# Kernel optimization log

Hardware: AMD Instinct MI355X
Metric: run time of the kernel (lower is better)

Reference implementation:

```python
import jax, jax.numpy as jnp
import numpy as np

# Module hyperparameters (from init_kwargs)
P = 96                 # num_of_patches
W = 1536.0             # input width
H = 1536.0             # input height
XPS = W / P            # x patch size = 16
YPS = H / P            # y patch size = 16
PROB_THR = 0.9
IOU_THR = 0.5
N = P * P              # total candidate boxes


def setup_inputs() -> dict:
    key = jax.random.key(0)
    # x: [5, P, P] -> channel 0 = probability, 1..4 = (x, y, w, h) in [0,1)
    x = jax.random.uniform(key, (5, P, P), dtype=jnp.float32)
    return {"x": x}


def _pairwise_iou(b):
    # b: [N, 4] xyxy
    x1, y1, x2, y2 = b[:, 0], b[:, 1], b[:, 2], b[:, 3]
    area = (x2 - x1) * (y2 - y1)                       # [N]
    ix1 = jnp.maximum(x1[:, None], x1[None, :])
    iy1 = jnp.maximum(y1[:, None], y1[None, :])
    ix2 = jnp.minimum(x2[:, None], x2[None, :])
    iy2 = jnp.minimum(y2[:, None], y2[None, :])
    inter = jnp.clip(ix2 - ix1, 0.0) * jnp.clip(iy2 - iy1, 0.0)
    union = area[:, None] + area[None, :] - inter
    return jnp.where(union > 0, inter / union, 0.0)    # [N, N]


def _forward(x):
    # --- scale_batch_bbx_xywh, applied densely (invalid entries are masked later) ---
    p = x[0]
    ii = jnp.arange(P, dtype=x.dtype)[:, None]   # row index i
    jj = jnp.arange(P, dtype=x.dtype)[None, :]   # col index j
    bx = x[1] * XPS + ii * XPS
    by = x[2] * YPS + jj * YPS
    bw = x[3] * W
    bh = x[4] * H
    bbx = jnp.stack([p, bx, by, bw, bh], axis=0).reshape(5, N).T   # [N, 5] (p, x, y, w, h)

    # --- remove_low_probability_bbx: fixed-shape validity mask instead of filtering ---
    scores = bbx[:, 0]
    valid = scores > PROB_THR

    # --- convert_batch_to_xyxy + round ---
    x1 = jnp.round(bbx[:, 1])
    y1 = jnp.round(bbx[:, 2])
    x2 = jnp.round(bbx[:, 3] + bbx[:, 1])
    y2 = jnp.round(bbx[:, 4] + bbx[:, 2])

    # --- greedy NMS (torchvision semantics): sort by score desc, suppress by IoU ---
    sort_key = jnp.where(valid, scores, -jnp.inf)
    order = jnp.argsort(-sort_key)
    boxes = jnp.stack([x1, y1, x2, y2], axis=1)[order]   # [N, 4] sorted
    sc = scores[order]
    v = valid[order]
    iou = _pairwise_iou(boxes)                           # [N, N]

    def body(kept, i):
        suppressed = jnp.any(kept & (iou[i] > IOU_THR))
        ki = v[i] & ~suppressed
        return kept.at[i].set(ki), ki

    _, keeps = jax.lax.scan(body, jnp.zeros((N,), bool), jnp.arange(N))

    # --- cat([scores, bbx]) then convert_batch_to_xywh on kept rows ---
    out = jnp.stack(
        [sc, boxes[:, 0], boxes[:, 1], boxes[:, 2] - boxes[:, 0], boxes[:, 3] - boxes[:, 1]],
        axis=1,
    )  # [N, 5] = (score, x, y, w, h), score-descending order like nms output
    out = jnp.where(keeps[:, None], out, 0.0)
    return out, keeps


def reference(x):
    # Returns (out [N,5], keep_mask [N]); rows with keep_mask=False are zeroed.
    # This is the fixed-shape equivalent of the variable-length torch output.
    return _forward(x)
```

## Files before the change

kernel.cpp:

```cpp
#include <hip/hip_runtime.h>

#define PP 96
#define NB (PP*PP)
#define NCH (NB/64)
#define PROB_THR 0.9f
#define FAST_CAP 1024
#define LSTRIDE 1034

typedef unsigned long long u64;
typedef unsigned int u32;

__device__ __forceinline__ void decode_core(int n, float xv, float yv, float wv, float hv,
                                            float& X1, float& Y1, float& X2, float& Y2)
{
    int i = n / PP;
    int j = n - i * PP;
    float bx = __fadd_rn(__fmul_rn(xv, 16.0f), (float)i * 16.0f);
    float by = __fadd_rn(__fmul_rn(yv, 16.0f), (float)j * 16.0f);
    float bw = __fmul_rn(wv, 1536.0f);
    float bh = __fmul_rn(hv, 1536.0f);
    X1 = rintf(bx);
    Y1 = rintf(by);
    X2 = rintf(__fadd_rn(bw, bx));
    Y2 = rintf(__fadd_rn(bh, by));
}

__device__ __forceinline__ void decode_box(const float* __restrict__ x, int n,
                                           float& X1, float& Y1, float& X2, float& Y2)
{
    decode_core(n, x[NB + n], x[2 * NB + n], x[3 * NB + n], x[4 * NB + n], X1, Y1, X2, Y2);
}

__device__ __forceinline__ int iou_hit_nodiv(float ix1, float iy1, float ix2, float iy2, float iar,
                                             float jx1, float jy1, float jx2, float jy2, float jar)
{
    float xx1 = fmaxf(ix1, jx1), yy1 = fmaxf(iy1, jy1);
    float xx2 = fminf(ix2, jx2), yy2 = fminf(iy2, jy2);
    float iw = fmaxf(__fsub_rn(xx2, xx1), 0.0f);
    float ih = fmaxf(__fsub_rn(yy2, yy1), 0.0f);
    float inter = __fmul_rn(iw, ih);
    float uni = __fsub_rn(__fadd_rn(iar, jar), inter);
    return (uni > 0.0f && __fadd_rn(inter, inter) > uni) ? 1 : 0;
}

__device__ __forceinline__ int iou_hit_div(float ix1, float iy1, float ix2, float iy2, float iar,
                                           float jx1, float jy1, float jx2, float jy2, float jar)
{
    float xx1 = fmaxf(ix1, jx1), yy1 = fmaxf(iy1, jy1);
    float xx2 = fminf(ix2, jx2), yy2 = fminf(iy2, jy2);
    float iw = fmaxf(__fsub_rn(xx2, xx1), 0.0f);
    float ih = fmaxf(__fsub_rn(yy2, yy1), 0.0f);
    float inter = __fmul_rn(iw, ih);
    float uni = __fsub_rn(__fadd_rn(iar, jar), inter);
    return (uni > 0.0f && __fdiv_rn(inter, uni) > 0.5f) ? 1 : 0;
}

__global__ void __launch_bounds__(256) k_sort(
    const float* __restrict__ x,
    float* __restrict__ gss, float4* __restrict__ gbox,
    u64* __restrict__ skeys, int* __restrict__ counter, int ws_ok)
{
    __shared__ u64 lmask[NCH];
    __shared__ int pc[NCH], loff[NCH];
    __shared__ int sM;
    __shared__ u64 kdb[FAST_CAP];
    __shared__ int prank[256];

    const int tid = threadIdx.x;
    const int lane = tid & 63;
    const int wv = tid >> 6;
    const int b = blockIdx.x;

    #pragma unroll
    for (int g = 0; g < 36; g += 6) {
        float sv[6];
        #pragma unroll
        for (int u = 0; u < 6; ++u)
            sv[u] = x[((wv * 36 + g + u) << 6) + lane];
        #pragma unroll
        for (int u = 0; u < 6; ++u) {
            u64 m = __ballot(sv[u] > PROB_THR);
            if (lane == 0) lmask[wv * 36 + g + u] = m;
        }
    }
    __syncthreads();
    if (tid < NCH) pc[tid] = __popcll(lmask[tid]);
    __syncthreads();
    if (tid < 64) {
        int acc = 0;
        for (int seg = 0; seg < 3; ++seg) {
            int c = (seg << 6) + lane;
            int pv = (c < NCH) ? pc[c] : 0;
            int v = pv;
            #pragma unroll
            for (int off = 1; off < 64; off <<= 1) {
                int u = __shfl_up(v, off);
                if (lane >= off) v += u;
            }
            if (c < NCH) loff[c] = acc + v - pv;
            acc += __shfl(v, 63);
        }
        if (lane == 0) sM = acc;
    }
    __syncthreads();
    const int M = sM;
    const bool fast = (M <= FAST_CAP) && ws_ok;
    if (b == 0 && tid == 0) counter[0] = M;

    if (!fast) {
        if (b == 0) {
            for (int c = wv; c < NCH; c += 4) {
                float s = x[(c << 6) + lane];
                u64 m = lmask[c];
                if ((m >> lane) & 1ull) {
                    int pos = loff[c] + __popcll(m & ((1ull << lane) - 1ull));
                    int n = (c << 6) + lane;
                    skeys[pos] = ((u64)__float_as_uint(s) << 32) | (u64)(NB - 1 - n);
                }
            }
        }
        return;
    }

    for (int c = wv; c < NCH; c += 4) {
        float s = x[(c << 6) + lane];
        u64 m = lmask[c];
        if ((m >> lane) & 1ull) {
            int pos = loff[c] + __popcll(m & ((1ull << lane) - 1ull));
            int n = (c << 6) + lane;
            kdb[pos] = ((u64)__float_as_uint(s) << 32) | (u64)(NB - 1 - n);
        }
    }
    for (int q = M + tid; q < FAST_CAP; q += 256) kdb[q] = 0ull;
    __syncthreads();

    const int cand = (b << 6) + lane;
    const u64 k0 = kdb[cand];
    const int n0 = NB - 1 - (int)(k0 & 0xFFFFFFFFull);
    float xv0 = x[NB + n0], yv0 = x[2 * NB + n0];
    float wv0 = x[3 * NB + n0], hv0 = x[4 * NB + n0];
    int r = 0;
    const int nck = (M + 63) >> 6;
    for (int ch = wv; ch < nck; ch += 4) {
        u64 kq = kdb[(ch << 6) + lane];
        u32 qlo = (u32)kq, qhi = (u32)(kq >> 32);
        #pragma unroll
        for (int i = 0; i < 64; ++i) {
            u32 blo = (u32)__builtin_amdgcn_readlane((int)qlo, i);
            u32 bhi = (u32)__builtin_amdgcn_readlane((int)qhi, i);
            u64 kb = ((u64)bhi << 32) | (u64)blo;
            r += (kb > k0) ? 1 : 0;
        }
    }
    prank[tid] = r;
    __syncthreads();
    if (tid < 64 && cand < M) {
        int rk = prank[tid] + prank[64 + tid] + prank[128 + tid] + prank[192 + tid];
        float X1, Y1, X2, Y2;
        decode_core(n0, xv0, yv0, wv0, hv0, X1, Y1, X2, Y2);
        gbox[rk] = make_float4(X1, Y1, X2, Y2);
        gss[rk] = __uint_as_float((u32)(k0 >> 32));
    }
}

__global__ void __launch_bounds__(256) k_adj(
    float* __restrict__ out, const float4* __restrict__ gbox,
    const int* __restrict__ counter, u64* __restrict__ adjT, int ws_ok)
{
    __shared__ float4 lb[FAST_CAP];
    __shared__ float la[FAST_CAP];
    int M = counter[0]; if (M > NB) M = NB;
    const int tid = threadIdx.x, lane = tid & 63, wv = tid >> 6, b = blockIdx.x;

    float4 z4 = make_float4(0.f, 0.f, 0.f, 0.f);
    for (int q = tid; q < 216; q += 256)
        ((float4*)out)[b * 216 + q] = z4;

    const bool fast = (M <= FAST_CAP) && ws_ok;
    if (!fast) return;
    if ((b << 4) >= M) return;

    const int W = (M + 63) >> 6;
    for (int f = tid; f < M; f += 256) {
        float4 bb = gbox[f];
        lb[f] = bb;
        la[f] = __fmul_rn(__fsub_rn(bb.z, bb.x), __fsub_rn(bb.w, bb.y));
    }
    __syncthreads();

    #pragma unroll
    for (int r = 0; r < 4; ++r) {
        int i = (b << 4) + (r << 2) + wv;
        if (i >= M) break;
        float4 bi = lb[i];
        float iar = la[i];
        for (int kk = 0; kk < W; ++kk) {
            int j = (kk << 6) + lane;
            float4 bj = lb[j & (FAST_CAP - 1)];
            float jar = la[j & (FAST_CAP - 1)];
            int hit = (j < M) && iou_hit_nodiv(bi.x, bi.y, bi.z, bi.w, iar,
                                               bj.x, bj.y, bj.z, bj.w, jar);
            u64 mm = __ballot(hit);
            if (lane == 0) adjT[((size_t)kk << 10) + i] = mm;
        }
    }
}

__global__ void __launch_bounds__(256) k_sweep(
    const float* __restrict__ x, float* __restrict__ out,
    float* __restrict__ gss, float4* __restrict__ gbox,
    const u64* __restrict__ skeys, const int* __restrict__ counter,
    const u64* __restrict__ adjT, int ws_ok)
{
    __shared__ __align__(16) u64 Lds[16 * LSTRIDE];
    __shared__ u64 keepw[NCH];
    int M = counter[0]; if (M > NB) M = NB;
    const int W = (M + 63) >> 6;
    const bool fast = (M <= FAST_CAP) && ws_ok;
    const int tid = threadIdx.x, lane = tid & 63;

    if (fast) {
        const int npair = W << 9;
        const ulonglong2* gp = (const ulonglong2*)adjT;
        for (int r = 0; r < 4; ++r) {
            int fb = (r << 11) + tid;
            ulonglong2 v[8];
            #pragma unroll
            for (int u = 0; u < 8; ++u) {
                int f = fb + (u << 8);
                v[u] = (f < npair) ? gp[f] : make_ulonglong2(0ull, 0ull);
            }
            #pragma unroll
            for (int u = 0; u < 8; ++u) {
                int f = fb + (u << 8);
                if (f < npair) {
                    int w = f >> 9, r2 = f & 511;
                    ((ulonglong2*)Lds)[w * (LSTRIDE >> 1) + r2] = v[u];
                }
            }
        }
        __syncthreads();

        if (tid < 64) {
            const int wl = (lane < W) ? lane : 0;
            u32 supl = 0u, suph = 0u, dl = 0u, dh = 0u;
            u64 mykw = 0ull;
            const int nrb = (M + 31) >> 5;
            for (int rb = 0; rb < nrb; ++rb) {
                const int c = rb >> 1;
                const int base = rb << 5;
                const ulonglong2* crow = (const ulonglong2*)(Lds + (size_t)c * LSTRIDE + base);
                const ulonglong2* rrow = (const ulonglong2*)(Lds + (size_t)wl * LSTRIDE + base);
                u64 colb[32], rowb[32];
                #pragma unroll
                for (int q = 0; q < 16; ++q) {
                    ulonglong2 t2 = crow[q];
                    colb[2 * q] = t2.x; colb[2 * q + 1] = t2.y;
                }
                #pragma unroll
                for (int q = 0; q < 16; ++q) {
                    ulonglong2 t2 = rrow[q];
                    rowb[2 * q] = t2.x; rowb[2 * q + 1] = t2.y;
                }
                if (!(rb & 1)) {
                    if (rb == 0) { dl = 0u; dh = 0u; }
                    else { dl = (u32)__shfl((int)supl, c); dh = (u32)__shfl((int)suph, c); }
                    int rem = M - (c << 6);
                    if (rem < 64) {
                        if (rem >= 32) dh |= 0xFFFFFFFFu << (rem - 32);
                        else { dh = 0xFFFFFFFFu; dl |= 0xFFFFFFFFu << rem; }
                    }
                }
                u32 kw = 0u;
                if (!(rb & 1)) {
                    #pragma unroll
                    for (int t = 0; t < 32; ++t) {
                        u32 bbit = (dl >> t) & 1u;
                        u32 m = bbit - 1u;
                        dl |= (u32)colb[t] & m;
                        dh |= (u32)(colb[t] >> 32) & m;
                        kw |= m & (1u << t);
                    }
                } else {
                    #pragma unroll
                    for (int t = 0; t < 32; ++t) {
                        u32 bbit = (dh >> t) & 1u;
                        u32 m = bbit - 1u;
                        dl |= (u32)colb[t] & m;
                        dh |= (u32)(colb[t] >> 32) & m;
                        kw |= m & (1u << t);
                    }
                }
                #pragma unroll
                for (int t = 0; t < 32; ++t) {
                    u32 m = 0u - ((kw >> t) & 1u);
                    supl |= (u32)rowb[t] & m;
                    suph |= (u32)(rowb[t] >> 32) & m;
                }
                mykw |= (lane == c) ? ((u64)kw << ((rb & 1) << 5)) : 0ull;
            }
            keepw[lane] = mykw;
        }
    } else {
        for (int t = tid; t < M; t += 256) {
            u64 key = skeys[t];
            int r = 0;
            for (int q = 0; q < M; ++q) r += (skeys[q] > key) ? 1 : 0;
            int n = NB - 1 - (int)(key & 0xFFFFFFFFull);
            float X1, Y1, X2, Y2;
            decode_box(x, n, X1, Y1, X2, Y2);
            gbox[r] = make_float4(X1, Y1, X2, Y2);
            gss[r] = __uint_as_float((u32)(key >> 32));
        }
        __threadfence();
        __syncthreads();
        if (tid < 64) {
            u64 kbs[3] = {0ull, 0ull, 0ull};
            for (int i = 0; i < M; ++i) {
                float4 bi = gbox[i];
                float iar = __fmul_rn(__fsub_rn(bi.z, bi.x), __fsub_rn(bi.w, bi.y));
                int hit = 0;
                int nk = (i > lane) ? ((i - lane + 63) >> 6) : 0;
                for (int w = 0; w < 3 && !hit; ++w) {
                    int klim = nk - (w << 6);
                    if (klim <= 0) break;
                    u64 bits = kbs[w];
                    if (klim < 64) bits &= ((1ull << klim) - 1ull);
                    while (bits) {
                        int kk2 = __builtin_ctzll(bits);
                        bits &= bits - 1ull;
                        int jj = lane + (((w << 6) + kk2) << 6);
                        float4 bj = gbox[jj];
                        float jar = __fmul_rn(__fsub_rn(bj.z, bj.x), __fsub_rn(bj.w, bj.y));
                        if (iou_hit_div(bi.x, bi.y, bi.z, bi.w, iar,
                                        bj.x, bj.y, bj.z, bj.w, jar)) { hit = 1; break; }
                    }
                }
                int suppressed = __any(hit);
                if (!suppressed && lane == (i & 63)) kbs[(i >> 6) >> 6] |= 1ull << ((i >> 6) & 63);
            }
            int NWrd = (M + 63) >> 6;
            for (int wd = 0; wd < NWrd; ++wd) {
                u64 bit = (kbs[wd >> 6] >> (wd & 63)) & 1ull;
                u64 word = __ballot(bit != 0);
                if (lane == 0 && wd < NCH) keepw[wd] = word;
            }
        }
    }
    __syncthreads();

    for (int i = tid; i < M; i += 256) {
        if ((keepw[i >> 6] >> (i & 63)) & 1ull) {
            float4 bb = gbox[i];
            out[i * 5 + 0] = gss[i];
            out[i * 5 + 1] = bb.x;
            out[i * 5 + 2] = bb.y;
            out[i * 5 + 3] = __fsub_rn(bb.z, bb.x);
            out[i * 5 + 4] = __fsub_rn(bb.w, bb.y);
            out[5 * NB + i] = 1.0f;
        }
    }
}

extern "C" void kernel_launch(void* const* d_in, const int* in_sizes, int n_in,
                              void* d_out, int out_size, void* d_ws, size_t ws_size,
                              hipStream_t stream) {
    const float* x = (const float*)d_in[0];
    float* out = (float*)d_out;

    char* ws = (char*)d_ws;
    int* counter = (int*)ws;
    float*  gss  = (float*)(ws + 16);
    float4* gbox = (float4*)(ws + 16 + (size_t)4 * NB);
    u64*    adjT = (u64*)(ws + 16 + (size_t)4 * NB + (size_t)16 * NB);
    u64*    skeys = (u64*)((char*)adjT + (size_t)16384 * 8);
    const size_t NEEDED = 16 + (size_t)4 * NB + (size_t)16 * NB
                        + (size_t)16384 * 8 + (size_t)8 * NB;
    int ws_ok = (ws_size >= NEEDED) ? 1 : 0;

    k_sort<<<16, 256, 0, stream>>>(x, gss, gbox, skeys, counter, ws_ok);
    k_adj<<<64, 256, 0, stream>>>(out, gbox, counter, adjT, ws_ok);
    k_sweep<<<1, 256, 0, stream>>>(x, out, gss, gbox, skeys, counter, adjT, ws_ok);
}
```

Measured before the change: 104.2 us.

## Fuse sort, adjacency and sweep kernels into one cooperative kernel

Merges the three launches into a single cooperative kernel of 64 blocks that uses grid.sync between phases. Blocks 0-15 rank-sort the candidates while blocks 16-63 zero the output, then all blocks build the adjacency bitmask, and block 0 runs the greedy sweep. Shared memory is overlaid through a union across the phases. The aim is to remove inter-kernel launch gaps, in exchange for the cost of cooperative launch and grid-wide barriers.

```diff
diff --git a/kernel.cpp b/kernel.cpp
--- a/kernel.cpp
+++ b/kernel.cpp
@@ -1,4 +1,7 @@
 #include <hip/hip_runtime.h>
+#include <hip/hip_cooperative_groups.h>
+
+namespace cg = cooperative_groups;
 
 #define PP 96
 #define NB (PP*PP)
@@ -55,170 +58,167 @@
     return (uni > 0.0f && __fdiv_rn(inter, uni) > 0.5f) ? 1 : 0;
 }
 
-__global__ void __launch_bounds__(256) k_sort(
-    const float* __restrict__ x,
+__global__ void __launch_bounds__(256, 1) k_fused(
+    const float* __restrict__ x, float* __restrict__ out,
     float* __restrict__ gss, float4* __restrict__ gbox,
-    u64* __restrict__ skeys, int* __restrict__ counter, int ws_ok)
-{
-    __shared__ u64 lmask[NCH];
-    __shared__ int pc[NCH], loff[NCH];
-    __shared__ int sM;
-    __shared__ u64 kdb[FAST_CAP];
-    __shared__ int prank[256];
+    u64* __restrict__ skeys, int* __restrict__ counter,
+    u64* __restrict__ adjT, int ws_ok)
+{
+    cg::grid_group grid = cg::this_grid();
+
+    __shared__ __align__(16) union ShU {
+        struct {
+            u64 lmask[NCH]; int pc[NCH]; int loff[NCH]; int sM;
+            u64 kdb[FAST_CAP]; int prank[256];
+        } a;
+        struct {
+            float4 lb[FAST_CAP]; float la[FAST_CAP];
+        } p2;
+        struct {
+            u64 Lds[16 * LSTRIDE]; u64 keepw[NCH];
+        } p3;
+    } sh;
 
     const int tid = threadIdx.x;
     const int lane = tid & 63;
     const int wv = tid >> 6;
     const int b = blockIdx.x;
 
-    #pragma unroll
-    for (int g = 0; g < 36; g += 6) {
-        float sv[6];
+    if (b < 16) {
         #pragma unroll
-        for (int u = 0; u < 6; ++u)
-            sv[u] = x[((wv * 36 + g + u) << 6) + lane];
-        #pragma unroll
-        for (int u = 0; u < 6; ++u) {
-            u64 m = __ballot(sv[u] > PROB_THR);
-            if (lane == 0) lmask[wv * 36 + g + u] = m;
-        }
-    }
-    __syncthreads();
-    if (tid < NCH) pc[tid] = __popcll(lmask[tid]);
-    __syncthreads();
-    if (tid < 64) {
-        int acc = 0;
-        for (int seg = 0; seg < 3; ++seg) {
-            int c = (seg << 6) + lane;
-            int pv = (c < NCH) ? pc[c] : 0;
-            int v = pv;
+        for (int g = 0; g < 36; g += 6) {
+            float sv[6];
             #pragma unroll
-            for (int off = 1; off < 64; off <<= 1) {
-                int u = __shfl_up(v, off);
-                if (lane >= off) v += u;
-            }
-            if (c < NCH) loff[c] = acc + v - pv;
-            acc += __shfl(v, 63);
-        }
-        if (lane == 0) sM = acc;
-    }
-    __syncthreads();
-    const int M = sM;
-    const bool fast = (M <= FAST_CAP) && ws_ok;
-    if (b == 0 && tid == 0) counter[0] = M;
-
-    if (!fast) {
-        if (b == 0) {
+            for (int u = 0; u < 6; ++u)
+                sv[u] = x[((wv * 36 + g + u) << 6) + lane];
+            #pragma unroll
+            for (int u = 0; u < 6; ++u) {
+                u64 m = __ballot(sv[u] > PROB_THR);
+                if (lane == 0) sh.a.lmask[wv * 36 + g + u] = m;
+            }
+        }
+        __syncthreads();
+        if (tid < NCH) sh.a.pc[tid] = __popcll(sh.a.lmask[tid]);
+        __syncthreads();
+        if (tid < 64) {
+            int acc = 0;
+            for (int seg = 0; seg < 3; ++seg) {
+                int c = (seg << 6) + lane;
+                int pv = (c < NCH) ? sh.a.pc[c] : 0;
+                int v = pv;
+                #pragma unroll
+                for (int off = 1; off < 64; off <<= 1) {
+                    int u = __shfl_up(v, off);
+                    if (lane >= off) v += u;
+                }
+                if (c < NCH) sh.a.loff[c] = acc + v - pv;
+                acc += __shfl(v, 63);
+            }
+            if (lane == 0) sh.a.sM = acc;
+        }
+        __syncthreads();
+        const int Ma = sh.a.sM;
+        const bool fasta = (Ma <= FAST_CAP) && ws_ok;
+        if (b == 0 && tid == 0) counter[0] = Ma;
+
+        if (!fasta) {
+            if (b == 0) {
+                for (int c = wv; c < NCH; c += 4) {
+                    float s = x[(c << 6) + lane];
+                    u64 m = sh.a.lmask[c];
+                    if ((m >> lane) & 1ull) {
+                        int pos = sh.a.loff[c] + __popcll(m & ((1ull << lane) - 1ull));
+                        int n = (c << 6) + lane;
+                        skeys[pos] = ((u64)__float_as_uint(s) << 32) | (u64)(NB - 1 - n);
+                    }
+                }
+            }
+        } else {
             for (int c = wv; c < NCH; c += 4) {
                 float s = x[(c << 6) + lane];
-                u64 m = lmask[c];
+                u64 m = sh.a.lmask[c];
                 if ((m >> lane) & 1ull) {
-                    int pos = loff[c] + __popcll(m & ((1ull << lane) - 1ull));
+                    int pos = sh.a.loff[c] + __popcll(m & ((1ull << lane) - 1ull));
                     int n = (c << 6) + lane;
-                    skeys[pos] = ((u64)__float_as_uint(s) << 32) | (u64)(NB - 1 - n);
-                }
-            }
-        }
-        return;
+                    sh.a.kdb[pos] = ((u64)__float_as_uint(s) << 32) | (u64)(NB - 1 - n);
+                }
+            }
+            for (int q = Ma + tid; q < FAST_CAP; q += 256) sh.a.kdb[q] = 0ull;
+            __syncthreads();
+
+            const int cand = (b << 6) + lane;
+            const u64 k0 = sh.a.kdb[cand];
+            const int n0 = NB - 1 - (int)(k0 & 0xFFFFFFFFull);
+            float xv0 = x[NB + n0], yv0 = x[2 * NB + n0];
+            float wv0 = x[3 * NB + n0], hv0 = x[4 * NB + n0];
+            int r = 0;
+            const int nck = (Ma + 63) >> 6;
+            for (int ch = wv; ch < nck; ch += 4) {
+                u64 kq = sh.a.kdb[(ch << 6) + lane];
+                u32 qlo = (u32)kq, qhi = (u32)(kq >> 32);
+                #pragma unroll
+                for (int i = 0; i < 64; ++i) {
+                    u32 blo = (u32)__builtin_amdgcn_readlane((int)qlo, i);
+                    u32 bhi = (u32)__builtin_amdgcn_readlane((int)qhi, i);
+                    u64 kb = ((u64)bhi << 32) | (u64)blo;
+                    r += (kb > k0) ? 1 : 0;
+                }
+            }
+            sh.a.prank[tid] = r;
+            __syncthreads();
+            if (tid < 64 && cand < Ma) {
+                int rk = sh.a.prank[tid] + sh.a.prank[64 + tid]
+                       + sh.a.prank[128 + tid] + sh.a.prank[192 + tid];
+                float X1, Y1, X2, Y2;
+                decode_core(n0, xv0, yv0, wv0, hv0, X1, Y1, X2, Y2);
+                gbox[rk] = make_float4(X1, Y1, X2, Y2);
+                gss[rk] = __uint_as_float((u32)(k0 >> 32));
+            }
+        }
+    } else {
+        float4 z4 = make_float4(0.f, 0.f, 0.f, 0.f);
+        const int base = (b - 16) * 288;
+        for (int q = tid; q < 288; q += 256)
+            ((float4*)out)[base + q] = z4;
     }
-
-    for (int c = wv; c < NCH; c += 4) {
-        float s = x[(c << 6) + lane];
-        u64 m = lmask[c];
-        if ((m >> lane) & 1ull) {
-            int pos = loff[c] + __popcll(m & ((1ull << lane) - 1ull));
-            int n = (c << 6) + lane;
-            kdb[pos] = ((u64)__float_as_uint(s) << 32) | (u64)(NB - 1 - n);
+    __threadfence();
+    grid.sync();
+
+    int M = *(volatile int*)counter; if (M > NB) M = NB;
+    const bool fast = (M <= FAST_CAP) && ws_ok;
+
+    if (fast && ((b << 4) < M)) {
+        const int W = (M + 63) >> 6;
+        for (int f = tid; f < M; f += 256) {
+            float4 bb = gbox[f];
+            sh.p2.lb[f] = bb;
+            sh.p2.la[f] = __fmul_rn(__fsub_rn(bb.z, bb.x), __fsub_rn(bb.w, bb.y));
+        }
+        __syncthreads();
+
+        #pragma unroll
+        for (int r = 0; r < 4; ++r) {
+            int i = (b << 4) + (r << 2) + wv;
+            if (i >= M) break;
+            float4 bi = sh.p2.lb[i];
+            float iar = sh.p2.la[i];
+            for (int kk = 0; kk < W; ++kk) {
+                int j = (kk << 6) + lane;
+                float4 bj = sh.p2.lb[j & (FAST_CAP - 1)];
+                float jar = sh.p2.la[j & (FAST_CAP - 1)];
+                int hit = (j < M) && iou_hit_nodiv(bi.x, bi.y, bi.z, bi.w, iar,
+                                                   bj.x, bj.y, bj.z, bj.w, jar);
+                u64 mm = __ballot(hit);
+                if (lane == 0) adjT[((size_t)kk << 10) + i] = mm;
+            }
         }
     }
-    for (int q = M + tid; q < FAST_CAP; q += 256) kdb[q] = 0ull;
-    __syncthreads();
-
-    const int cand = (b << 6) + lane;
-    const u64 k0 = kdb[cand];
-    const int n0 = NB - 1 - (int)(k0 & 0xFFFFFFFFull);
-    float xv0 = x[NB + n0], yv0 = x[2 * NB + n0];
-    float wv0 = x[3 * NB + n0], hv0 = x[4 * NB + n0];
-    int r = 0;
-    const int nck = (M + 63) >> 6;
-    for (int ch = wv; ch < nck; ch += 4) {
-        u64 kq = kdb[(ch << 6) + lane];
-        u32 qlo = (u32)kq, qhi = (u32)(kq >> 32);
-        #pragma unroll
-        for (int i = 0; i < 64; ++i) {
-            u32 blo = (u32)__builtin_amdgcn_readlane((int)qlo, i);
-            u32 bhi = (u32)__builtin_amdgcn_readlane((int)qhi, i);
-            u64 kb = ((u64)bhi << 32) | (u64)blo;
-            r += (kb > k0) ? 1 : 0;
-        }
-    }
-    prank[tid] = r;
-    __syncthreads();
-    if (tid < 64 && cand < M) {
-        int rk = prank[tid] + prank[64 + tid] + prank[128 + tid] + prank[192 + tid];
-        float X1, Y1, X2, Y2;
-        decode_core(n0, xv0, yv0, wv0, hv0, X1, Y1, X2, Y2);
-        gbox[rk] = make_float4(X1, Y1, X2, Y2);
-        gss[rk] = __uint_as_float((u32)(k0 >> 32));
-    }
-}
-
-__global__ void __launch_bounds__(256) k_adj(
-    float* __restrict__ out, const float4* __restrict__ gbox,
-    const int* __restrict__ counter, u64* __restrict__ adjT, int ws_ok)
-{
-    __shared__ float4 lb[FAST_CAP];
-    __shared__ float la[FAST_CAP];
-    int M = counter[0]; if (M > NB) M = NB;
-    const int tid = threadIdx.x, lane = tid & 63, wv = tid >> 6, b = blockIdx.x;
-
-    float4 z4 = make_float4(0.f, 0.f, 0.f, 0.f);
-    for (int q = tid; q < 216; q += 256)
-        ((float4*)out)[b * 216 + q] = z4;
-
-    const bool fast = (M <= FAST_CAP) && ws_ok;
-    if (!fast) return;
-    if ((b << 4) >= M) return;
+    __threadfence();
+    grid.sync();
+
+    if (b != 0) return;
 
     const int W = (M + 63) >> 6;
-    for (int f = tid; f < M; f += 256) {
-        float4 bb = gbox[f];
-        lb[f] = bb;
-        la[f] = __fmul_rn(__fsub_rn(bb.z, bb.x), __fsub_rn(bb.w, bb.y));
-    }
-    __syncthreads();
-
-    #pragma unroll
-    for (int r = 0; r < 4; ++r) {
-        int i = (b << 4) + (r << 2) + wv;
-        if (i >= M) break;
-        float4 bi = lb[i];
-        float iar = la[i];
-        for (int kk = 0; kk < W; ++kk) {
-            int j = (kk << 6) + lane;
-            float4 bj = lb[j & (FAST_CAP - 1)];
-            float jar = la[j & (FAST_CAP - 1)];
-            int hit = (j < M) && iou_hit_nodiv(bi.x, bi.y, bi.z, bi.w, iar,
-                                               bj.x, bj.y, bj.z, bj.w, jar);
-            u64 mm = __ballot(hit);
-            if (lane == 0) adjT[((size_t)kk << 10) + i] = mm;
-        }
-    }
-}
-
-__global__ void __launch_bounds__(256) k_sweep(
-    const float* __restrict__ x, float* __restrict__ out,
-    float* __restrict__ gss, float4* __restrict__ gbox,
-    const u64* __restrict__ skeys, const int* __restrict__ counter,
-    const u64* __restrict__ adjT, int ws_ok)
-{
-    __shared__ __align__(16) u64 Lds[16 * LSTRIDE];
-    __shared__ u64 keepw[NCH];
-    int M = counter[0]; if (M > NB) M = NB;
-    const int W = (M + 63) >> 6;
-    const bool fast = (M <= FAST_CAP) && ws_ok;
-    const int tid = threadIdx.x, lane = tid & 63;
-
     if (fast) {
         const int npair = W << 9;
         const ulonglong2* gp = (const ulonglong2*)adjT;
@@ -235,7 +235,7 @@
                 int f = fb + (u << 8);
                 if (f < npair) {
                     int w = f >> 9, r2 = f & 511;
-                    ((ulonglong2*)Lds)[w * (LSTRIDE >> 1) + r2] = v[u];
+                    ((ulonglong2*)sh.p3.Lds)[w * (LSTRIDE >> 1) + r2] = v[u];
                 }
             }
         }
@@ -249,8 +249,8 @@
             for (int rb = 0; rb < nrb; ++rb) {
                 const int c = rb >> 1;
                 const int base = rb << 5;
-                const ulonglong2* crow = (const ulonglong2*)(Lds + (size_t)c * LSTRIDE + base);
-                const ulonglong2* rrow = (const ulonglong2*)(Lds + (size_t)wl * LSTRIDE + base);
+                const ulonglong2* crow = (const ulonglong2*)(sh.p3.Lds + (size_t)c * LSTRIDE + base);
+                const ulonglong2* rrow = (const ulonglong2*)(sh.p3.Lds + (size_t)wl * LSTRIDE + base);
                 u64 colb[32], rowb[32];
                 #pragma unroll
                 for (int q = 0; q < 16; ++q) {
@@ -299,7 +299,7 @@
                 }
                 mykw |= (lane == c) ? ((u64)kw << ((rb & 1) << 5)) : 0ull;
             }
-            keepw[lane] = mykw;
+            sh.p3.keepw[lane] = mykw;
         }
     } else {
         for (int t = tid; t < M; t += 256) {
@@ -343,14 +343,14 @@
             for (int wd = 0; wd < NWrd; ++wd) {
                 u64 bit = (kbs[wd >> 6] >> (wd & 63)) & 1ull;
                 u64 word = __ballot(bit != 0);
-                if (lane == 0 && wd < NCH) keepw[wd] = word;
+                if (lane == 0 && wd < NCH) sh.p3.keepw[wd] = word;
             }
         }
     }
     __syncthreads();
 
     for (int i = tid; i < M; i += 256) {
-        if ((keepw[i >> 6] >> (i & 63)) & 1ull) {
+        if ((sh.p3.keepw[i >> 6] >> (i & 63)) & 1ull) {
             float4 bb = gbox[i];
             out[i * 5 + 0] = gss[i];
             out[i * 5 + 1] = bb.x;
@@ -378,7 +378,8 @@
                         + (size_t)16384 * 8 + (size_t)8 * NB;
     int ws_ok = (ws_size >= NEEDED) ? 1 : 0;
 
-    k_sort<<<16, 256, 0, stream>>>(x, gss, gbox, skeys, counter, ws_ok);
-    k_adj<<<64, 256, 0, stream>>>(out, gbox, counter, adjT, ws_ok);
-    k_sweep<<<1, 256, 0, stream>>>(x, out, gss, gbox, skeys, counter, adjT, ws_ok);
-}
+    void* kargs[] = { (void*)&x, (void*)&out, (void*)&gss, (void*)&gbox,
+                      (void*)&skeys, (void*)&counter, (void*)&adjT, (void*)&ws_ok };
+    hipLaunchCooperativeKernel(reinterpret_cast<void*>(&k_fused),
+                               dim3(64), dim3(256), kargs, 0, stream);
+}
```

After: 145.6 us. 1.4x slower.

## Fuse rank-sort and IoU adjacency kernels into one redundant-sort front kernel

Applied to the files above, without the earlier changes.

Merges the sort kernel and the adjacency kernel into a single 64-block launch. Every block recomputes the full rank sort of all candidates (each thread ranks four candidates) and keeps the sorted boxes in LDS, so there is no global round trip through gbox and one kernel launch is removed. Block 0 still writes the sorted boxes and scores for the sweep, and zeroing of the output moves into the single-block sweep kernel. The cost is redundant sort work in every block plus a serial zero-fill of the whole output by one block.

```diff
diff --git a/kernel.cpp b/kernel.cpp
--- a/kernel.cpp
+++ b/kernel.cpp
@@ -55,16 +55,18 @@
     return (uni > 0.0f && __fdiv_rn(inter, uni) > 0.5f) ? 1 : 0;
 }
 
-__global__ void __launch_bounds__(256) k_sort(
+__global__ void __launch_bounds__(256) k_front(
     const float* __restrict__ x,
     float* __restrict__ gss, float4* __restrict__ gbox,
-    u64* __restrict__ skeys, int* __restrict__ counter, int ws_ok)
+    u64* __restrict__ skeys, int* __restrict__ counter,
+    u64* __restrict__ adjT, int ws_ok)
 {
     __shared__ u64 lmask[NCH];
     __shared__ int pc[NCH], loff[NCH];
     __shared__ int sM;
     __shared__ u64 kdb[FAST_CAP];
-    __shared__ int prank[256];
+    __shared__ float4 lb[FAST_CAP];
+    __shared__ float la[FAST_CAP];
 
     const int tid = threadIdx.x;
     const int lane = tid & 63;
@@ -121,6 +123,7 @@
         }
         return;
     }
+    if (b != 0 && (b << 4) >= M) return;
 
     for (int c = wv; c < NCH; c += 4) {
         float s = x[(c << 6) + lane];
@@ -134,14 +137,20 @@
     for (int q = M + tid; q < FAST_CAP; q += 256) kdb[q] = 0ull;
     __syncthreads();
 
-    const int cand = (b << 6) + lane;
-    const u64 k0 = kdb[cand];
-    const int n0 = NB - 1 - (int)(k0 & 0xFFFFFFFFull);
-    float xv0 = x[NB + n0], yv0 = x[2 * NB + n0];
-    float wv0 = x[3 * NB + n0], hv0 = x[4 * NB + n0];
-    int r = 0;
+    u64 k0v[4]; int rkv[4]; int n0v[4];
+    float xvv[4], yvv[4], wvv[4], hvv[4];
+    #pragma unroll
+    for (int g = 0; g < 4; ++g) {
+        k0v[g] = kdb[(g << 8) + tid];
+        rkv[g] = 0;
+        n0v[g] = NB - 1 - (int)(k0v[g] & 0xFFFFFFFFull);
+        xvv[g] = x[NB + n0v[g]];
+        yvv[g] = x[2 * NB + n0v[g]];
+        wvv[g] = x[3 * NB + n0v[g]];
+        hvv[g] = x[4 * NB + n0v[g]];
+    }
     const int nck = (M + 63) >> 6;
-    for (int ch = wv; ch < nck; ch += 4) {
+    for (int ch = 0; ch < nck; ++ch) {
         u64 kq = kdb[(ch << 6) + lane];
         u32 qlo = (u32)kq, qhi = (u32)(kq >> 32);
         #pragma unroll
@@ -149,45 +158,31 @@
             u32 blo = (u32)__builtin_amdgcn_readlane((int)qlo, i);
             u32 bhi = (u32)__builtin_amdgcn_readlane((int)qhi, i);
             u64 kb = ((u64)bhi << 32) | (u64)blo;
-            r += (kb > k0) ? 1 : 0;
-        }
-    }
-    prank[tid] = r;
-    __syncthreads();
-    if (tid < 64 && cand < M) {
-        int rk = prank[tid] + prank[64 + tid] + prank[128 + tid] + prank[192 + tid];
-        float X1, Y1, X2, Y2;
-        decode_core(n0, xv0, yv0, wv0, hv0, X1, Y1, X2, Y2);
-        gbox[rk] = make_float4(X1, Y1, X2, Y2);
-        gss[rk] = __uint_as_float((u32)(k0 >> 32));
-    }
-}
-
-__global__ void __launch_bounds__(256) k_adj(
-    float* __restrict__ out, const float4* __restrict__ gbox,
-    const int* __restrict__ counter, u64* __restrict__ adjT, int ws_ok)
-{
-    __shared__ float4 lb[FAST_CAP];
-    __shared__ float la[FAST_CAP];
-    int M = counter[0]; if (M > NB) M = NB;
-    const int tid = threadIdx.x, lane = tid & 63, wv = tid >> 6, b = blockIdx.x;
-
-    float4 z4 = make_float4(0.f, 0.f, 0.f, 0.f);
-    for (int q = tid; q < 216; q += 256)
-        ((float4*)out)[b * 216 + q] = z4;
-
-    const bool fast = (M <= FAST_CAP) && ws_ok;
-    if (!fast) return;
-    if ((b << 4) >= M) return;
+            #pragma unroll
+            for (int g = 0; g < 4; ++g)
+                rkv[g] += (kb > k0v[g]) ? 1 : 0;
+        }
+    }
+
+    #pragma unroll
+    for (int g = 0; g < 4; ++g) {
+        int cand = (g << 8) + tid;
+        if (cand < M) {
+            float X1, Y1, X2, Y2;
+            decode_core(n0v[g], xvv[g], yvv[g], wvv[g], hvv[g], X1, Y1, X2, Y2);
+            float4 bb = make_float4(X1, Y1, X2, Y2);
+            int rk = rkv[g];
+            lb[rk] = bb;
+            la[rk] = __fmul_rn(__fsub_rn(X2, X1), __fsub_rn(Y2, Y1));
+            if (b == 0) {
+                gbox[rk] = bb;
+                gss[rk] = __uint_as_float((u32)(k0v[g] >> 32));
+            }
+        }
+    }
+    __syncthreads();
 
     const int W = (M + 63) >> 6;
-    for (int f = tid; f < M; f += 256) {
-        float4 bb = gbox[f];
-        lb[f] = bb;
-        la[f] = __fmul_rn(__fsub_rn(bb.z, bb.x), __fsub_rn(bb.w, bb.y));
-    }
-    __syncthreads();
-
     #pragma unroll
     for (int r = 0; r < 4; ++r) {
         int i = (b << 4) + (r << 2) + wv;
@@ -214,10 +209,18 @@
 {
     __shared__ __align__(16) u64 Lds[16 * LSTRIDE];
     __shared__ u64 keepw[NCH];
+
+    const int tid = threadIdx.x, lane = tid & 63;
+
+    {
+        float4 z4 = make_float4(0.f, 0.f, 0.f, 0.f);
+        for (int q = tid; q < 13824; q += 256)
+            ((float4*)out)[q] = z4;
+    }
+
     int M = counter[0]; if (M > NB) M = NB;
     const int W = (M + 63) >> 6;
     const bool fast = (M <= FAST_CAP) && ws_ok;
-    const int tid = threadIdx.x, lane = tid & 63;
 
     if (fast) {
         const int npair = W << 9;
@@ -378,7 +381,6 @@
                         + (size_t)16384 * 8 + (size_t)8 * NB;
     int ws_ok = (ws_size >= NEEDED) ? 1 : 0;
 
-    k_sort<<<16, 256, 0, stream>>>(x, gss, gbox, skeys, counter, ws_ok);
-    k_adj<<<64, 256, 0, stream>>>(out, gbox, counter, adjT, ws_ok);
+    k_front<<<64, 256, 0, stream>>>(x, gss, gbox, skeys, counter, adjT, ws_ok);
     k_sweep<<<1, 256, 0, stream>>>(x, out, gss, gbox, skeys, counter, adjT, ws_ok);
 }
```

Measured after the change: 120.1 us. 1.15x slower.

## Fuse adjacency and sweep kernels with flag-based streaming of adjacency tiles

Applied to the files above, without the earlier changes.

Merges the adjacency-building kernel and the single-block greedy sweep into one launch. Block 0 runs the sweep and waits on per-group release/acquire flags, while the other 64 blocks compute adjacency rows. Block 0 streams 32-row tiles into a double-buffered LDS region, so the sweep can start before the whole matrix is finished and one kernel launch is removed. Output zeroing moves into the sort kernel. The risks are spin-wait overhead, a __syncthreads on every row block of the sweep, and a possible deadlock if the block that spins is scheduled before the producer blocks can run.

```diff
diff --git a/kernel.cpp b/kernel.cpp
--- a/kernel.cpp
+++ b/kernel.cpp
@@ -5,7 +5,6 @@
 #define NCH (NB/64)
 #define PROB_THR 0.9f
 #define FAST_CAP 1024
-#define LSTRIDE 1034
 
 typedef unsigned long long u64;
 typedef unsigned int u32;
@@ -56,9 +55,10 @@
 }
 
 __global__ void __launch_bounds__(256) k_sort(
-    const float* __restrict__ x,
+    const float* __restrict__ x, float* __restrict__ out,
     float* __restrict__ gss, float4* __restrict__ gbox,
-    u64* __restrict__ skeys, int* __restrict__ counter, int ws_ok)
+    u64* __restrict__ skeys, int* __restrict__ counter,
+    u32* __restrict__ flags, int ws_ok)
 {
     __shared__ u64 lmask[NCH];
     __shared__ int pc[NCH], loff[NCH];
@@ -70,6 +70,13 @@
     const int lane = tid & 63;
     const int wv = tid >> 6;
     const int b = blockIdx.x;
+
+    {
+        float4 z4 = make_float4(0.f, 0.f, 0.f, 0.f);
+        for (int q = tid; q < 864; q += 256)
+            ((float4*)out)[b * 864 + q] = z4;
+        if (b == 0 && tid < 64) flags[tid] = 0u;
+    }
 
     #pragma unroll
     for (int g = 0; g < 36; g += 6) {
@@ -163,144 +170,172 @@
     }
 }
 
-__global__ void __launch_bounds__(256) k_adj(
-    float* __restrict__ out, const float4* __restrict__ gbox,
-    const int* __restrict__ counter, u64* __restrict__ adjT, int ws_ok)
-{
-    __shared__ float4 lb[FAST_CAP];
-    __shared__ float la[FAST_CAP];
-    int M = counter[0]; if (M > NB) M = NB;
-    const int tid = threadIdx.x, lane = tid & 63, wv = tid >> 6, b = blockIdx.x;
-
-    float4 z4 = make_float4(0.f, 0.f, 0.f, 0.f);
-    for (int q = tid; q < 216; q += 256)
-        ((float4*)out)[b * 216 + q] = z4;
-
-    const bool fast = (M <= FAST_CAP) && ws_ok;
-    if (!fast) return;
-    if ((b << 4) >= M) return;
-
-    const int W = (M + 63) >> 6;
-    for (int f = tid; f < M; f += 256) {
-        float4 bb = gbox[f];
-        lb[f] = bb;
-        la[f] = __fmul_rn(__fsub_rn(bb.z, bb.x), __fsub_rn(bb.w, bb.y));
-    }
-    __syncthreads();
-
-    #pragma unroll
-    for (int r = 0; r < 4; ++r) {
-        int i = (b << 4) + (r << 2) + wv;
-        if (i >= M) break;
-        float4 bi = lb[i];
-        float iar = la[i];
-        for (int kk = 0; kk < W; ++kk) {
-            int j = (kk << 6) + lane;
-            float4 bj = lb[j & (FAST_CAP - 1)];
-            float jar = la[j & (FAST_CAP - 1)];
-            int hit = (j < M) && iou_hit_nodiv(bi.x, bi.y, bi.z, bi.w, iar,
-                                               bj.x, bj.y, bj.z, bj.w, jar);
-            u64 mm = __ballot(hit);
-            if (lane == 0) adjT[((size_t)kk << 10) + i] = mm;
-        }
-    }
-}
-
-__global__ void __launch_bounds__(256) k_sweep(
+__global__ void __launch_bounds__(256) k_adjsweep(
     const float* __restrict__ x, float* __restrict__ out,
     float* __restrict__ gss, float4* __restrict__ gbox,
     const u64* __restrict__ skeys, const int* __restrict__ counter,
-    const u64* __restrict__ adjT, int ws_ok)
-{
-    __shared__ __align__(16) u64 Lds[16 * LSTRIDE];
-    __shared__ u64 keepw[NCH];
+    u64* __restrict__ adjT, u32* __restrict__ flags, int ws_ok)
+{
+    __shared__ __align__(16) union ShU {
+        struct { float4 lb[FAST_CAP]; float la[FAST_CAP]; } p;
+        struct { u64 buf[2][16][34]; u64 keepw[NCH]; } c;
+    } sh;
+
+    const int tid = threadIdx.x, lane = tid & 63, wv = tid >> 6;
+    const int b = blockIdx.x;
+
     int M = counter[0]; if (M > NB) M = NB;
+    const bool fast = (M <= FAST_CAP) && ws_ok;
     const int W = (M + 63) >> 6;
-    const bool fast = (M <= FAST_CAP) && ws_ok;
-    const int tid = threadIdx.x, lane = tid & 63;
+
+    if (b != 0) {
+        const int g = b - 1;
+        if (!fast) return;
+        if ((g << 4) >= M) {
+            if (tid == 0)
+                __hip_atomic_store(&flags[g], 1u, __ATOMIC_RELEASE, __HIP_MEMORY_SCOPE_AGENT);
+            return;
+        }
+        for (int f = tid; f < M; f += 256) {
+            float4 bb = gbox[f];
+            sh.p.lb[f] = bb;
+            sh.p.la[f] = __fmul_rn(__fsub_rn(bb.z, bb.x), __fsub_rn(bb.w, bb.y));
+        }
+        __syncthreads();
+        #pragma unroll
+        for (int r = 0; r < 4; ++r) {
+            int i = (g << 4) + (r << 2) + wv;
+            if (i >= M) break;
+            float4 bi = sh.p.lb[i];
+            float iar = sh.p.la[i];
+            for (int kk = 0; kk < W; ++kk) {
+                int j = (kk << 6) + lane;
+                float4 bj = sh.p.lb[j & (FAST_CAP - 1)];
+                float jar = sh.p.la[j & (FAST_CAP - 1)];
+                int hit = (j < M) && iou_hit_nodiv(bi.x, bi.y, bi.z, bi.w, iar,
+                                                   bj.x, bj.y, bj.z, bj.w, jar);
+                u64 mm = __ballot(hit);
+                if (lane == 0) adjT[((size_t)kk << 10) + i] = mm;
+            }
+        }
+        __syncthreads();
+        if (tid == 0) {
+            __threadfence();
+            __hip_atomic_store(&flags[g], 1u, __ATOMIC_RELEASE, __HIP_MEMORY_SCOPE_AGENT);
+        }
+        return;
+    }
 
     if (fast) {
-        const int npair = W << 9;
-        const ulonglong2* gp = (const ulonglong2*)adjT;
-        for (int r = 0; r < 4; ++r) {
-            int fb = (r << 11) + tid;
-            ulonglong2 v[8];
-            #pragma unroll
-            for (int u = 0; u < 8; ++u) {
-                int f = fb + (u << 8);
-                v[u] = (f < npair) ? gp[f] : make_ulonglong2(0ull, 0ull);
-            }
-            #pragma unroll
-            for (int u = 0; u < 8; ++u) {
-                int f = fb + (u << 8);
-                if (f < npair) {
-                    int w = f >> 9, r2 = f & 511;
-                    ((ulonglong2*)Lds)[w * (LSTRIDE >> 1) + r2] = v[u];
+        const int nrb = (M + 31) >> 5;
+        const int ngroups = (M + 15) >> 4;
+        const int wl = (lane < W) ? lane : 0;
+        const ulonglong2* gp2 = (const ulonglong2*)adjT;
+
+        u32 supl = 0u, suph = 0u, dl = 0u, dh = 0u;
+        u64 mykw = 0ull;
+
+        if (nrb > 0) {
+            {
+                int w = tid >> 4, tt = tid & 15;
+                int g = tt >> 3;
+                if (g < ngroups) {
+                    while (__hip_atomic_load(&flags[g], __ATOMIC_ACQUIRE,
+                                             __HIP_MEMORY_SCOPE_AGENT) == 0u)
+                        __builtin_amdgcn_s_sleep(2);
                 }
-            }
-        }
-        __syncthreads();
-
-        if (tid < 64) {
-            const int wl = (lane < W) ? lane : 0;
-            u32 supl = 0u, suph = 0u, dl = 0u, dh = 0u;
-            u64 mykw = 0ull;
-            const int nrb = (M + 31) >> 5;
+                ulonglong2 v = gp2[(w << 9) | tt];
+                *(ulonglong2*)&sh.c.buf[0][w][2 * tt] = v;
+            }
+            __syncthreads();
+
             for (int rb = 0; rb < nrb; ++rb) {
-                const int c = rb >> 1;
-                const int base = rb << 5;
-                const ulonglong2* crow = (const ulonglong2*)(Lds + (size_t)c * LSTRIDE + base);
-                const ulonglong2* rrow = (const ulonglong2*)(Lds + (size_t)wl * LSTRIDE + base);
-                u64 colb[32], rowb[32];
-                #pragma unroll
-                for (int q = 0; q < 16; ++q) {
-                    ulonglong2 t2 = crow[q];
-                    colb[2 * q] = t2.x; colb[2 * q + 1] = t2.y;
-                }
-                #pragma unroll
-                for (int q = 0; q < 16; ++q) {
-                    ulonglong2 t2 = rrow[q];
-                    rowb[2 * q] = t2.x; rowb[2 * q + 1] = t2.y;
-                }
-                if (!(rb & 1)) {
-                    if (rb == 0) { dl = 0u; dh = 0u; }
-                    else { dl = (u32)__shfl((int)supl, c); dh = (u32)__shfl((int)suph, c); }
-                    int rem = M - (c << 6);
-                    if (rem < 64) {
-                        if (rem >= 32) dh |= 0xFFFFFFFFu << (rem - 32);
-                        else { dh = 0xFFFFFFFFu; dl |= 0xFFFFFFFFu << rem; }
-                    }
-                }
-                u32 kw = 0u;
-                if (!(rb & 1)) {
+                const int pbi = rb & 1;
+                const int rbn = rb + 1;
+                if (tid >= 64) {
+                    if (rbn < nrb) {
+                        const int p2a = tid - 64;
+                        const int wA = p2a >> 4, ttA = p2a & 15;
+                        const int gA = (rbn << 1) + (ttA >> 3);
+                        if (gA < ngroups) {
+                            while (__hip_atomic_load(&flags[gA], __ATOMIC_ACQUIRE,
+                                                     __HIP_MEMORY_SCOPE_AGENT) == 0u)
+                                __builtin_amdgcn_s_sleep(2);
+                        }
+                        ulonglong2 va = gp2[(wA << 9) | ((rbn << 4) + ttA)];
+                        const int p2b = p2a + 192;
+                        const bool hasB = (p2b < 256);
+                        int wB = 0, ttB = 0;
+                        ulonglong2 vb = make_ulonglong2(0ull, 0ull);
+                        if (hasB) {
+                            wB = p2b >> 4; ttB = p2b & 15;
+                            const int gB = (rbn << 1) + (ttB >> 3);
+                            if (gB < ngroups) {
+                                while (__hip_atomic_load(&flags[gB], __ATOMIC_ACQUIRE,
+                                                         __HIP_MEMORY_SCOPE_AGENT) == 0u)
+                                    __builtin_amdgcn_s_sleep(2);
+                            }
+                            vb = gp2[(wB << 9) | ((rbn << 4) + ttB)];
+                        }
+                        *(ulonglong2*)&sh.c.buf[pbi ^ 1][wA][2 * ttA] = va;
+                        if (hasB) *(ulonglong2*)&sh.c.buf[pbi ^ 1][wB][2 * ttB] = vb;
+                    }
+                } else {
+                    const int c = rb >> 1;
+                    const ulonglong2* crow = (const ulonglong2*)&sh.c.buf[pbi][c][0];
+                    const ulonglong2* rrow = (const ulonglong2*)&sh.c.buf[pbi][wl][0];
+                    u64 colb[32], rowb[32];
+                    #pragma unroll
+                    for (int q = 0; q < 16; ++q) {
+                        ulonglong2 t2 = crow[q];
+                        colb[2 * q] = t2.x; colb[2 * q + 1] = t2.y;
+                    }
+                    #pragma unroll
+                    for (int q = 0; q < 16; ++q) {
+                        ulonglong2 t2 = rrow[q];
+                        rowb[2 * q] = t2.x; rowb[2 * q + 1] = t2.y;
+                    }
+                    if (!(rb & 1)) {
+                        if (rb == 0) { dl = 0u; dh = 0u; }
+                        else { dl = (u32)__shfl((int)supl, c); dh = (u32)__shfl((int)suph, c); }
+                        int rem = M - (c << 6);
+                        if (rem < 64) {
+                            if (rem >= 32) dh |= 0xFFFFFFFFu << (rem - 32);
+                            else { dh = 0xFFFFFFFFu; dl |= 0xFFFFFFFFu << rem; }
+                        }
+                    }
+                    u32 kw = 0u;
+                    if (!(rb & 1)) {
+                        #pragma unroll
+                        for (int t = 0; t < 32; ++t) {
+                            u32 bbit = (dl >> t) & 1u;
+                            u32 m = bbit - 1u;
+                            dl |= (u32)colb[t] & m;
+                            dh |= (u32)(colb[t] >> 32) & m;
+                            kw |= m & (1u << t);
+                        }
+                    } else {
+                        #pragma unroll
+                        for (int t = 0; t < 32; ++t) {
+                            u32 bbit = (dh >> t) & 1u;
+                            u32 m = bbit - 1u;
+                            dl |= (u32)colb[t] & m;
+                            dh |= (u32)(colb[t] >> 32) & m;
+                            kw |= m & (1u << t);
+                        }
+                    }
                     #pragma unroll
                     for (int t = 0; t < 32; ++t) {
-                        u32 bbit = (dl >> t) & 1u;
-                        u32 m = bbit - 1u;
-                        dl |= (u32)colb[t] & m;
-                        dh |= (u32)(colb[t] >> 32) & m;
-                        kw |= m & (1u << t);
-                    }
-                } else {
-                    #pragma unroll
-                    for (int t = 0; t < 32; ++t) {
-                        u32 bbit = (dh >> t) & 1u;
-                        u32 m = bbit - 1u;
-                        dl |= (u32)colb[t] & m;
-                        dh |= (u32)(colb[t] >> 32) & m;
-                        kw |= m & (1u << t);
-                    }
+                        u32 m = 0u - ((kw >> t) & 1u);
+                        supl |= (u32)rowb[t] & m;
+                        suph |= (u32)(rowb[t] >> 32) & m;
+                    }
+                    mykw |= (lane == c) ? ((u64)kw << ((rb & 1) << 5)) : 0ull;
                 }
-                #pragma unroll
-                for (int t = 0; t < 32; ++t) {
-                    u32 m = 0u - ((kw >> t) & 1u);
-                    supl |= (u32)rowb[t] & m;
-                    suph |= (u32)(rowb[t] >> 32) & m;
-                }
-                mykw |= (lane == c) ? ((u64)kw << ((rb & 1) << 5)) : 0ull;
-            }
-            keepw[lane] = mykw;
-        }
+                __syncthreads();
+            }
+        }
+        if (tid < 64) sh.c.keepw[lane] = mykw;
     } else {
         for (int t = tid; t < M; t += 256) {
             u64 key = skeys[t];
@@ -343,14 +378,14 @@
             for (int wd = 0; wd < NWrd; ++wd) {
                 u64 bit = (kbs[wd >> 6] >> (wd & 63)) & 1ull;
                 u64 word = __ballot(bit != 0);
-                if (lane == 0 && wd < NCH) keepw[wd] = word;
+                if (lane == 0 && wd < NCH) sh.c.keepw[wd] = word;
             }
         }
     }
     __syncthreads();
 
     for (int i = tid; i < M; i += 256) {
-        if ((keepw[i >> 6] >> (i & 63)) & 1ull) {
+        if ((sh.c.keepw[i >> 6] >> (i & 63)) & 1ull) {
             float4 bb = gbox[i];
             out[i * 5 + 0] = gss[i];
             out[i * 5 + 1] = bb.x;
@@ -374,11 +409,11 @@
     float4* gbox = (float4*)(ws + 16 + (size_t)4 * NB);
     u64*    adjT = (u64*)(ws + 16 + (size_t)4 * NB + (size_t)16 * NB);
     u64*    skeys = (u64*)((char*)adjT + (size_t)16384 * 8);
+    u32*    flags = (u32*)((char*)skeys + (size_t)8 * NB);
     const size_t NEEDED = 16 + (size_t)4 * NB + (size_t)16 * NB
-                        + (size_t)16384 * 8 + (size_t)8 * NB;
+                        + (size_t)16384 * 8 + (size_t)8 * NB + 256;
     int ws_ok = (ws_size >= NEEDED) ? 1 : 0;
 
-    k_sort<<<16, 256, 0, stream>>>(x, gss, gbox, skeys, counter, ws_ok);
-    k_adj<<<64, 256, 0, stream>>>(out, gbox, counter, adjT, ws_ok);
-    k_sweep<<<1, 256, 0, stream>>>(x, out, gss, gbox, skeys, counter, adjT, ws_ok);
-}
+    k_sort<<<16, 256, 0, stream>>>(x, out, gss, gbox, skeys, counter, flags, ws_ok);
+    k_adjsweep<<<65, 256, 0, stream>>>(x, out, gss, gbox, skeys, counter, adjT, flags, ws_ok);
+}
```

After: 113.3 us. +8.8%, slower.
